# Kernel optimization log

Measured on AMD Instinct MI355X. Metric: run time of the kernel, lower is better.

The kernel has to match this reference:

```python
import jax, jax.numpy as jnp
import numpy as np

B, E, F, Q = 8, 2000, 6000, 20
D = 256   # entity_dim == word_dim (required: word_embedding output feeds LSTM with input_size=word_dim)
WD = 256
L = 3
NUM_ENTITY, NUM_REL, NUM_WORD = 400000, 6000, 60000
NNZ = 2 * B * F
PAGERANK_LAMBDA, FACT_SCALE = 0.8, 3.0
VERY_NEG = -100000000000.0
VERY_SMALL = 1e-10


def _lin(x, W, b):
    return x @ W.T + b


def _sparse_bmm(indices, values, x, num_rows):
    # indices: [3, nnz] = (batch, row, col); x: [B, C, Dx] -> out [B, num_rows, Dx]
    b, r, c = indices[0], indices[1], indices[2]
    contrib = values[:, None] * x[b, c]
    seg = b * num_rows + r
    out = jax.ops.segment_sum(contrib, seg, num_segments=x.shape[0] * num_rows)
    return out.reshape(x.shape[0], num_rows, x.shape[2])


def _lstm(x, Wih, Whh, bih, bhh):
    # PyTorch LSTM, batch_first, 1 layer, unidirectional; gate order i,f,g,o
    Bb, T, _ = x.shape
    H = Whh.shape[1]
    def step(carry, xt):
        h, c = carry
        g = xt @ Wih.T + bih + h @ Whh.T + bhh
        i, f, gg, o = jnp.split(g, 4, axis=-1)
        c = jax.nn.sigmoid(f) * c + jax.nn.sigmoid(i) * jnp.tanh(gg)
        h = jax.nn.sigmoid(o) * jnp.tanh(c)
        return (h, c), h
    init = (jnp.zeros((Bb, H), x.dtype), jnp.zeros((Bb, H), x.dtype))
    (h, c), hs = jax.lax.scan(step, init, jnp.swapaxes(x, 0, 1))
    return jnp.swapaxes(hs, 0, 1), h


def setup_inputs():
    key = jax.random.key(0)
    ks = iter(jax.random.split(key, 48))
    p = lambda shape: jax.random.normal(next(ks), shape, jnp.float32) * 0.02
    inp = {}
    inp['local_entity'] = jax.random.randint(next(ks), (B, E), 0, NUM_ENTITY + 1)
    inp['q2e_adj_mat'] = (jax.random.uniform(next(ks), (B, E, 1)) < 0.01).astype(jnp.float32)
    inp['kb_fact_rel'] = jax.random.randint(next(ks), (B, F), 0, NUM_REL)
    inp['query_text'] = jax.random.randint(next(ks), (B, Q), 0, NUM_WORD)
    inp['answer_dist'] = (jax.random.uniform(next(ks), (B, E)) < 0.005).astype(jnp.float32)
    eb = jax.random.randint(next(ks), (NNZ,), 0, B)
    ef = jax.random.randint(next(ks), (NNZ,), 0, F)
    ee = jax.random.randint(next(ks), (NNZ,), 0, E)
    inp['e2f_indices'] = jnp.stack([eb, ef, ee])
    inp['e2f_val'] = jnp.ones((NNZ,), jnp.float32)
    fb = jax.random.randint(next(ks), (NNZ,), 0, B)
    fe = jax.random.randint(next(ks), (NNZ,), 0, E)
    ff = jax.random.randint(next(ks), (NNZ,), 0, F)
    inp['f2e_indices'] = jnp.stack([fb, fe, ff])
    inp['f2e_val'] = jnp.ones((NNZ,), jnp.float32)
    inp['entity_table'] = p((NUM_ENTITY + 1, WD)).at[-1].set(0.0)
    inp['ent_lin_W'] = p((D, WD)); inp['ent_lin_b'] = jnp.zeros((D,), jnp.float32)
    inp['relation_table'] = p((NUM_REL + 1, WD)).at[-1].set(0.0)
    inp['rel_lin_W'] = p((D, WD)); inp['rel_lin_b'] = jnp.zeros((D,), jnp.float32)
    inp['word_table'] = p((NUM_WORD + 1, D)).at[-1].set(0.0)
    inp['lstm_Wih'] = p((4 * D, WD)); inp['lstm_Whh'] = p((4 * D, D))
    inp['lstm_bih'] = jnp.zeros((4 * D,), jnp.float32); inp['lstm_bhh'] = jnp.zeros((4 * D,), jnp.float32)
    inp['q2e_W'] = p((L, D, D)); inp['q2e_b'] = jnp.zeros((L, D), jnp.float32)
    inp['e2q_W'] = p((L, D, 3 * D)); inp['e2q_b'] = jnp.zeros((L, D), jnp.float32)
    inp['e2e_W'] = p((L, D, 3 * D)); inp['e2e_b'] = jnp.zeros((L, D), jnp.float32)
    inp['head_W'] = p((L, D, D)); inp['head_b'] = jnp.zeros((L, D), jnp.float32)
    inp['tail_W'] = p((L, D, D)); inp['tail_b'] = jnp.zeros((L, D), jnp.float32)
    inp['self_W'] = p((L, D, D)); inp['self_b'] = jnp.zeros((L, D), jnp.float32)
    inp['score_W'] = p((1, D)); inp['score_b'] = jnp.zeros((1,), jnp.float32)
    return inp


def reference(local_entity, q2e_adj_mat, kb_fact_rel, query_text, answer_dist, e2f_indices, e2f_val, f2e_indices, f2e_val, entity_table, ent_lin_W, ent_lin_b, relation_table, rel_lin_W, rel_lin_b, word_table, lstm_Wih, lstm_Whh, lstm_bih, lstm_bhh, q2e_W, q2e_b, e2q_W, e2q_b, e2e_W, e2e_b, head_W, head_b, tail_W, tail_b, self_W, self_b, score_W, score_b):
    query_mask = (query_text != NUM_WORD).astype(jnp.float32)          # [B,Q]
    local_entity_mask = (local_entity != NUM_ENTITY).astype(jnp.float32)
    # query encoder (dropout = identity in eval)
    query_hidden, h_last = _lstm(word_table[query_text], lstm_Wih, lstm_Whh, lstm_bih, lstm_bhh)
    query_node_emb = h_last[:, None, :]                                # [B,1,D]
    local_fact_emb = _lin(relation_table[kb_fact_rel], rel_lin_W, rel_lin_b)  # [B,F,D]
    div = jnp.sqrt(jnp.float32(D))
    sim = jnp.einsum('bqd,bfd->bqf', query_hidden, local_fact_emb) / div
    sim = jax.nn.softmax(sim + (1.0 - query_mask)[:, :, None] * VERY_NEG, axis=1)
    att = jnp.einsum('bqf,bqd->bfd', sim, query_hidden)
    Wt = jnp.sum(att * local_fact_emb, axis=2) / div                   # [B,F]
    W_tilde = jnp.exp(Wt - jnp.max(Wt, axis=1, keepdims=True))
    e2fT = jnp.stack([e2f_indices[0], e2f_indices[2], e2f_indices[1]])  # transpose(1,2)
    e2f_softmax = _sparse_bmm(e2fT, e2f_val, W_tilde[:, :, None], E)[..., 0]
    e2f_softmax = jnp.maximum(e2f_softmax, VERY_SMALL)
    pagerank_f = q2e_adj_mat[..., 0]                                    # [B,E]
    local_entity_emb = _lin(entity_table[local_entity], ent_lin_W, ent_lin_b)  # [B,E,D]
    for i in range(L):
        q2e_emb = jnp.broadcast_to(_lin(query_node_emb, q2e_W[i], q2e_b[i]), (B, E, D))
        nxt = jnp.concatenate([local_entity_emb, q2e_emb], axis=2)
        e2f_emb = jax.nn.relu(_lin(local_fact_emb, self_W[i], self_b[i]) + _sparse_bmm(e2f_indices, e2f_val, _lin(local_entity_emb, head_W[i], head_b[i]), F))
        e2f_norm = W_tilde[:, :, None] * _sparse_bmm(e2f_indices, e2f_val, (pagerank_f / e2f_softmax)[:, :, None], F)
        e2f_emb = e2f_emb * e2f_norm
        f2e_emb = jax.nn.relu(_lin(local_entity_emb, self_W[i], self_b[i]) + _sparse_bmm(f2e_indices, f2e_val, _lin(e2f_emb, tail_W[i], tail_b[i]), E))
        pagerank_f = PAGERANK_LAMBDA * _sparse_bmm(f2e_indices, f2e_val, e2f_norm, E)[..., 0] + (1.0 - PAGERANK_LAMBDA) * pagerank_f
        nxt = jnp.concatenate([nxt, FACT_SCALE * f2e_emb], axis=2)      # [B,E,3D]
        query_node_emb = jnp.einsum('be,bed->bd', pagerank_f, _lin(nxt, e2q_W[i], e2q_b[i]))[:, None, :]
        local_entity_emb = jax.nn.relu(_lin(nxt, e2e_W[i], e2e_b[i]))
    score = _lin(local_entity_emb, score_W, score_b)[..., 0]            # [B,E]
    loss = jnp.mean(jnp.maximum(score, 0.0) - score * answer_dist + jnp.log1p(jnp.exp(-jnp.abs(score))))
    score_m = score + (1.0 - local_entity_mask) * VERY_NEG
    pred = jnp.argmax(score_m, axis=1)
    pred_dist = jax.nn.sigmoid(score_m) * local_entity_mask
    return (loss, pred, pred_dist)
```

## Files before the change

### kernel.cpp

```cpp
#include <hip/hip_runtime.h>
#include <math.h>

#define BB 8
#define EE 2000
#define FF 6000
#define QQ 20
#define DD 256
#define NENT 400000
#define NWORD 60000
#define NNZ_ 96000
#define VNEG  (-1e11f)
#define VSMALL 1e-10f

typedef __attribute__((ext_vector_type(8))) short short8v;
typedef __attribute__((ext_vector_type(4))) short short4v;
typedef __attribute__((ext_vector_type(4))) float f32x4;

__device__ __forceinline__ unsigned short f2bf_rne(float x)
{
    unsigned u = __float_as_uint(x);
    u += 0x7FFFu + ((u >> 16) & 1u);
    return (unsigned short)(u >> 16);
}
__device__ __forceinline__ float bf2f(unsigned short h)
{
    return __uint_as_float((unsigned)h << 16);
}

template<int GATHER, int DUALW, int RELU, int RS, int BIASB>
__device__ __forceinline__ void mgemm_body(
    const float* __restrict__ A1, const int* __restrict__ idx,
    const float* __restrict__ A2, float sA2,
    const short* __restrict__ W1h, const short* __restrict__ W1l,
    const short* __restrict__ W2h, const short* __restrict__ W2l,
    const float* __restrict__ biasA,
    const float* __restrict__ rowscale, const float* __restrict__ bias2,
    float* __restrict__ out, int by, int bx,
    short* __restrict__ Ah, short* __restrict__ Al)
{
    const int tid = threadIdx.x;
    const int lane = tid & 63, wv = tid >> 6;
    const int wrow = wv >> 1, wcol = wv & 1;
    const int row0 = by * 128, col0 = bx * 128;

    const int sr = tid >> 1;
    const int sko = (tid & 1) << 5;
    const int grow = row0 + sr;
    const float* aRow1 = GATHER ? A1 + (size_t)idx[grow] * 256 : A1 + (size_t)grow * 256;
    const float* aRow2 = DUALW ? A2 + (size_t)grow * 256 : nullptr;

    f32x4 acc[4][4];
    #pragma unroll
    for (int i = 0; i < 4; ++i)
        #pragma unroll
        for (int j = 0; j < 4; ++j) acc[i][j] = (f32x4){0.f, 0.f, 0.f, 0.f};

    const int nch = DUALW ? 8 : 4;
    for (int ch = 0; ch < nch; ++ch) {
        const bool hi2 = DUALW && (ch >= 4);
        const float* ar = hi2 ? aRow2 : aRow1;
        const int kbase = (ch & 3) << 6;
        #pragma unroll
        for (int q = 0; q < 8; ++q) {
            const int kc = sko + (q << 2);
            float4 a = *(const float4*)(ar + kbase + kc);
            if (DUALW && hi2) { a.x *= sA2; a.y *= sA2; a.z *= sA2; a.w *= sA2; }
            unsigned short h0 = f2bf_rne(a.x), h1 = f2bf_rne(a.y),
                           h2 = f2bf_rne(a.z), h3 = f2bf_rne(a.w);
            unsigned short l0 = f2bf_rne(a.x - bf2f(h0)), l1 = f2bf_rne(a.y - bf2f(h1)),
                           l2 = f2bf_rne(a.z - bf2f(h2)), l3 = f2bf_rne(a.w - bf2f(h3));
            const int tI = ((sr >> 4) << 1) + (kc >> 5);
            const int off = (tI << 9) + ((((sr & 15)) + (((kc >> 3) & 3) << 4)) << 3) + (kc & 7);
            *(short4v*)(Ah + off) = (short4v){(short)h0, (short)h1, (short)h2, (short)h3};
            *(short4v*)(Al + off) = (short4v){(short)l0, (short)l1, (short)l2, (short)l3};
        }
        __syncthreads();
        const short* Wh = hi2 ? W2h : W1h;
        const short* Wl = hi2 ? W2l : W1l;
        #pragma unroll
        for (int ks = 0; ks < 2; ++ks) {
            const int kg = kbase + (ks << 5) + ((lane >> 4) << 3);
            short8v bh[4], bl[4];
            #pragma unroll
            for (int ct = 0; ct < 4; ++ct) {
                const int c = col0 + (wcol << 6) + (ct << 4) + (lane & 15);
                bh[ct] = *(const short8v*)(Wh + (size_t)c * 256 + kg);
                bl[ct] = *(const short8v*)(Wl + (size_t)c * 256 + kg);
            }
            #pragma unroll
            for (int rt = 0; rt < 4; ++rt) {
                const int tI = (((wrow << 2) + rt) << 1) + ks;
                const short8v avh = *(const short8v*)(Ah + (tI << 9) + (lane << 3));
                const short8v avl = *(const short8v*)(Al + (tI << 9) + (lane << 3));
                #pragma unroll
                for (int ct = 0; ct < 4; ++ct) {
                    acc[rt][ct] = __builtin_amdgcn_mfma_f32_16x16x32_bf16(avh, bh[ct], acc[rt][ct], 0, 0, 0);
                    acc[rt][ct] = __builtin_amdgcn_mfma_f32_16x16x32_bf16(avh, bl[ct], acc[rt][ct], 0, 0, 0);
                    acc[rt][ct] = __builtin_amdgcn_mfma_f32_16x16x32_bf16(avl, bh[ct], acc[rt][ct], 0, 0, 0);
                }
            }
        }
        __syncthreads();
    }
    #pragma unroll
    for (int rt = 0; rt < 4; ++rt) {
        const int rb = row0 + (wrow << 6) + (rt << 4) + ((lane >> 4) << 2);
        #pragma unroll
        for (int ct = 0; ct < 4; ++ct) {
            const int c = col0 + (wcol << 6) + (ct << 4) + (lane & 15);
            #pragma unroll
            for (int j = 0; j < 4; ++j) {
                const int r = rb + j;
                float v = acc[rt][ct][j];
                v += BIASB ? biasA[(size_t)(r / EE) * 256 + c] : biasA[c];
                if (RS) v += rowscale[r] * bias2[c];
                if (RELU) v = fmaxf(v, 0.f);
                out[(size_t)r * 256 + c] = v;
            }
        }
    }
}

template<int GATHER, int DUALW, int RELU, int RS, int BIASB>
__global__ __launch_bounds__(256, 2) void mgemm_k(
    const float* __restrict__ A1, const int* __restrict__ idx,
    const float* __restrict__ A2, float sA2,
    const short* __restrict__ W1h, const short* __restrict__ W1l,
    const short* __restrict__ W2h, const short* __restrict__ W2l,
    const float* __restrict__ biasA,
    const float* __restrict__ rowscale, const float* __restrict__ bias2,
    float* __restrict__ out)
{
    __shared__ short Ah[16 * 512];
    __shared__ short Al[16 * 512];
    mgemm_body<GATHER, DUALW, RELU, RS, BIASB>(A1, idx, A2, sA2, W1h, W1l, W2h, W2l,
        biasA, rowscale, bias2, out, blockIdx.y, blockIdx.x, Ah, Al);
}

template<int GATHER>
__global__ __launch_bounds__(256, 2) void mgemm_pair_k(
    const float* __restrict__ Aa, const int* __restrict__ idxA,
    const short* __restrict__ Wah, const short* __restrict__ Wal,
    const float* __restrict__ ba, float* __restrict__ outa, int nya,
    const float* __restrict__ Ab, const int* __restrict__ idxB,
    const short* __restrict__ Wbh, const short* __restrict__ Wbl,
    const float* __restrict__ bb, float* __restrict__ outb)
{
    __shared__ short Ah[16 * 512];
    __shared__ short Al[16 * 512];
    const int by = blockIdx.y;
    if (by < nya)
        mgemm_body<GATHER, 0, 0, 0, 0>(Aa, idxA, nullptr, 1.f, Wah, Wal, nullptr, nullptr,
            ba, nullptr, nullptr, outa, by, blockIdx.x, Ah, Al);
    else
        mgemm_body<GATHER, 0, 0, 0, 0>(Ab, idxB, nullptr, 1.f, Wbh, Wbl, nullptr, nullptr,
            bb, nullptr, nullptr, outb, by - nya, blockIdx.x, Ah, Al);
}

__global__ void wpack_k(const float* __restrict__ relW, const float* __restrict__ entW,
                        const float* __restrict__ headW, const float* __restrict__ tailW,
                        const float* __restrict__ selfW, const float* __restrict__ e2eW,
                        short* __restrict__ wh, short* __restrict__ wl)
{
    int id = blockIdx.x * 256 + threadIdx.x;
    if (id >= 17 * 65536) return;
    int m = id >> 16, e = id & 65535;
    float x;
    if (m == 0)       x = relW[e];
    else if (m == 1)  x = entW[e];
    else if (m < 5)   x = headW[(size_t)(m - 2) * 65536 + e];
    else if (m < 8)   x = tailW[(size_t)(m - 5) * 65536 + e];
    else if (m < 11)  x = selfW[(size_t)(m - 8) * 65536 + e];
    else if (m < 14)  x = e2eW[(size_t)(m - 11) * 196608 + (size_t)(e >> 8) * 768 + (e & 255)];
    else              x = e2eW[(size_t)(m - 14) * 196608 + (size_t)(e >> 8) * 768 + 512 + (e & 255)];
    unsigned short h = f2bf_rne(x);
    wh[id] = (short)h;
    wl[id] = (short)f2bf_rne(x - bf2f(h));
}

template<int GATHER>
__global__ __launch_bounds__(256, 4) void gemm3_k(
    const float* __restrict__ A1, const int* __restrict__ idx,
    const float* __restrict__ W1, int ldw1,
    const float* __restrict__ biasA,
    float* __restrict__ out, int M, int N)
{
    __shared__ float As[16][68];
    __shared__ float Bs[16][132];
    const int tid = threadIdx.x;
    const int row0 = blockIdx.y * 64, col0 = blockIdx.x * 128;
    const int tx = tid & 15, ty = tid >> 4;
    const int srA = tid >> 2, skA = (tid & 3) << 2;
    const int srB = tid >> 1, skB = (tid & 1) << 3;
    const int grA = row0 + srA;
    const bool rvalid = (grA < M);
    const float* aRow1 = nullptr;
    if (rvalid) aRow1 = GATHER ? A1 + (size_t)idx[grA] * 256 : A1 + (size_t)grA * 256;
    const float* wR1 = W1 + (size_t)(col0 + srB) * ldw1;

    float acc[4][8];
    #pragma unroll
    for (int i = 0; i < 4; ++i)
        #pragma unroll
        for (int j = 0; j < 8; ++j) acc[i][j] = 0.f;

    float4 a0, b0, b1;
    auto fetch = [&](int ch) {
        const int k0 = ch << 4;
        if (rvalid) a0 = *(const float4*)(aRow1 + k0 + skA);
        else        a0 = make_float4(0.f, 0.f, 0.f, 0.f);
        b0 = *(const float4*)(wR1 + k0 + skB);
        b1 = *(const float4*)(wR1 + k0 + skB + 4);
    };

    fetch(0);
    for (int ch = 0; ch < 16; ++ch) {
        As[skA + 0][srA] = a0.x; As[skA + 1][srA] = a0.y;
        As[skA + 2][srA] = a0.z; As[skA + 3][srA] = a0.w;
        Bs[skB + 0][srB] = b0.x; Bs[skB + 1][srB] = b0.y;
        Bs[skB + 2][srB] = b0.z; Bs[skB + 3][srB] = b0.w;
        Bs[skB + 4][srB] = b1.x; Bs[skB + 5][srB] = b1.y;
        Bs[skB + 6][srB] = b1.z; Bs[skB + 7][srB] = b1.w;
        __syncthreads();
        if (ch + 1 < 16) fetch(ch + 1);
        #pragma unroll
        for (int kk = 0; kk < 16; ++kk) {
            float av[4], bv[8];
            *(float4*)&av[0] = *(const float4*)&As[kk][ty << 2];
            *(float4*)&bv[0] = *(const float4*)&Bs[kk][tx << 2];
            *(float4*)&bv[4] = *(const float4*)&Bs[kk][(tx << 2) + 64];
            #pragma unroll
            for (int i = 0; i < 4; ++i)
                #pragma unroll
                for (int j = 0; j < 8; ++j) acc[i][j] += av[i] * bv[j];
        }
        __syncthreads();
    }
    #pragma unroll
    for (int i = 0; i < 4; ++i) {
        int r = row0 + (ty << 2) + i;
        if (r >= M) continue;
        float* orow = out + (size_t)r * N;
        #pragma unroll
        for (int jh = 0; jh < 2; ++jh) {
            const int c = col0 + (jh << 6) + (tx << 2);
            float4 v;
            v.x = acc[i][jh * 4 + 0] + biasA[c + 0];
            v.y = acc[i][jh * 4 + 1] + biasA[c + 1];
            v.z = acc[i][jh * 4 + 2] + biasA[c + 2];
            v.w = acc[i][jh * 4 + 3] + biasA[c + 3];
            *(float4*)(orow + c) = v;
        }
    }
}

__global__ void csr_count2_k(const int* __restrict__ idxA, int* __restrict__ cntA,
                             const int* __restrict__ idxB, int* __restrict__ cntB)
{
    int k = blockIdx.x * 256 + threadIdx.x;
    if (k >= NNZ_) return;
    if (blockIdx.y == 0) atomicAdd(&cntA[idxA[k] * FF + idxA[NNZ_ + k]], 1);
    else                 atomicAdd(&cntB[idxB[k] * EE + idxB[NNZ_ + k]], 1);
}

__global__ __launch_bounds__(1024) void scan2_k(
    const int* __restrict__ cntA, int* __restrict__ rpA, int* __restrict__ curA, int nA,
    const int* __restrict__ cntB, int* __restrict__ rpB, int* __restrict__ curB, int nB)
{
    const int* cnt = blockIdx.x ? cntB : cntA;
    int* rp  = blockIdx.x ? rpB  : rpA;
    int* cur = blockIdx.x ? curB : curA;
    int n    = blockIdx.x ? nB   : nA;
    __shared__ int sums[1024];
    int t = threadIdx.x;
    int chunk = (n + 1023) / 1024;
    int lo = t * chunk, hi = lo + chunk;
    if (lo > n) lo = n;
    if (hi > n) hi = n;
    int s = 0;
    for (int i = lo; i < hi; ++i) s += cnt[i];
    sums[t] = s;
    __syncthreads();
    for (int off = 1; off < 1024; off <<= 1) {
        int v = (t >= off) ? sums[t - off] : 0;
        __syncthreads();
        sums[t] += v;
        __syncthreads();
    }
    int run = (t == 0) ? 0 : sums[t - 1];
    for (int i = lo; i < hi; ++i) { rp[i] = run; cur[i] = run; run += cnt[i]; }
    if (hi == n) rp[n] = run;
}

__global__ void csr_fill2_k(
    const int* __restrict__ idxA, const float* __restrict__ valA,
    int* __restrict__ curA, int* __restrict__ colA, float* __restrict__ vpA,
    const int* __restrict__ idxB, const float* __restrict__ valB,
    int* __restrict__ curB, int* __restrict__ colB, float* __restrict__ vpB)
{
    int k = blockIdx.x * 256 + threadIdx.x;
    if (k >= NNZ_) return;
    if (blockIdx.y == 0) {
        int row = idxA[k] * FF + idxA[NNZ_ + k];
        int p = atomicAdd(&curA[row], 1);
        colA[p] = idxA[2 * NNZ_ + k];
        vpA[p] = valA[k];
    } else {
        int row = idxB[k] * EE + idxB[NNZ_ + k];
        int p = atomicAdd(&curB[row], 1);
        colB[p] = idxB[2 * NNZ_ + k];
        vpB[p] = valB[k];
    }
}

__global__ void degw_k(const int* __restrict__ rp, const float* __restrict__ vp,
                       float* __restrict__ degw, int n)
{
    int r = blockIdx.x * 256 + threadIdx.x;
    if (r >= n) return;
    float s = 0.f;
    for (int j = rp[r]; j < rp[r + 1]; ++j) s += vp[j];
    degw[r] = s;
}

__global__ __launch_bounds__(256) void gather_fused_e2f_k(
    const int* __restrict__ rowptr, const int* __restrict__ col,
    const float* __restrict__ valp, const float* __restrict__ headsrc,
    const float* __restrict__ pr, const float* __restrict__ sm,
    const float* __restrict__ Wtil, float* __restrict__ e2fnrm,
    float* __restrict__ dst, int nrows)
{
    int gid = blockIdx.x * 256 + threadIdx.x;
    int row = gid >> 6, lane = gid & 63;
    if (row >= nrows) return;
    int b = row / FF;
    const float* prb = pr + (size_t)b * EE;
    const float* smb = sm + (size_t)b * EE;
    float4* dp = (float4*)(dst + (size_t)row * DD + (lane << 2));
    float4 acc = *dp;
    float ns = 0.f;
    int j0 = rowptr[row], j1 = rowptr[row + 1];
    for (int j = j0; j < j1; ++j) {
        int c = col[j];
        float v = valp[j];
        float4 x = *(const float4*)(headsrc + ((size_t)b * EE + c) * DD + (lane << 2));
        acc.x += v * x.x; acc.y += v * x.y; acc.z += v * x.z; acc.w += v * x.w;
        ns += v * (prb[c] / fmaxf(smb[c], VSMALL));
    }
    float nrm = Wtil[row] * ns;
    if (lane == 0) e2fnrm[row] = nrm;
    acc.x = fmaxf(acc.x, 0.f) * nrm; acc.y = fmaxf(acc.y, 0.f) * nrm;
    acc.z = fmaxf(acc.z, 0.f) * nrm; acc.w = fmaxf(acc.w, 0.f) * nrm;
    *dp = acc;
}

__global__ __launch_bounds__(256) void gather_sum_k(
    const int* __restrict__ rowptr, const int* __restrict__ col,
    const float* __restrict__ valp, const float* __restrict__ src,
    float* __restrict__ dst, int nrows, int nrPerB, int ncs)
{
    int gid = blockIdx.x * 256 + threadIdx.x;
    int row = gid >> 6, lane = gid & 63;
    if (row >= nrows) return;
    int b = row / nrPerB;
    float4 acc = make_float4(0.f, 0.f, 0.f, 0.f);
    int j0 = rowptr[row], j1 = rowptr[row + 1];
    for (int j = j0; j < j1; ++j) {
        int c = col[j];
        float v = valp[j];
        float4 x = *(const float4*)(src + ((size_t)b * ncs + c) * DD + (lane << 2));
        acc.x += v * x.x; acc.y += v * x.y; acc.z += v * x.z; acc.w += v * x.w;
    }
    *(float4*)(dst + (size_t)row * DD + (lane << 2)) = acc;
}

__global__ void transpose_whh_k(const float* __restrict__ Whh, float* __restrict__ WhhT)
{
    int i = blockIdx.x * 256 + threadIdx.x;
    int k = i >> 10, j = i & 1023;
    WhhT[i] = Whh[(size_t)j * 256 + k];
}

__global__ __launch_bounds__(256) void lstm_k(
    const float* __restrict__ Xg, const float* __restrict__ WhhT,
    const float* __restrict__ bhh, float* __restrict__ qh, float* __restrict__ qne)
{
    __shared__ float h[DD];
    __shared__ float gs[4 * DD];
    const int b = blockIdx.x, t = threadIdx.x;
    h[t] = 0.f;
    float c = 0.f;
    const float4 bb4 = *(const float4*)(bhh + 4 * t);
    const float4* wt4 = (const float4*)WhhT + t;
    __syncthreads();
    for (int step = 0; step < QQ; ++step) {
        float a0 = 0.f, a1 = 0.f, a2 = 0.f, a3 = 0.f;
        #pragma unroll 16
        for (int k = 0; k < DD; ++k) {
            float4 w = wt4[k * 256];
            float hk = h[k];
            a0 += w.x * hk; a1 += w.y * hk; a2 += w.z * hk; a3 += w.w * hk;
        }
        float4 xg = *(const float4*)(Xg + ((size_t)b * QQ + step) * 1024 + 4 * t);
        float4 g4 = make_float4(a0 + xg.x + bb4.x, a1 + xg.y + bb4.y,
                                a2 + xg.z + bb4.z, a3 + xg.w + bb4.w);
        *(float4*)(gs + 4 * t) = g4;
        __syncthreads();
        float gi = gs[t], gf = gs[DD + t], gg = gs[2 * DD + t], go = gs[3 * DD + t];
        float si = 1.f / (1.f + expf(-gi));
        float sf = 1.f / (1.f + expf(-gf));
        float so = 1.f / (1.f + expf(-go));
        c = sf * c + si * tanhf(gg);
        float hh = so * tanhf(c);
        h[t] = hh;
        qh[((size_t)b * QQ + step) * DD + t] = hh;
        __syncthreads();
    }
    qne[(size_t)b * DD + t] = h[t];
}

__global__ __launch_bounds__(256) void simwt_k(
    const float* __restrict__ qhid, const int* __restrict__ qtext,
    const float* __restrict__ lfe, float* __restrict__ Wt)
{
    __shared__ float qs[QQ * DD];
    __shared__ float qmn[QQ];
    const int b = blockIdx.y;
    const int f = blockIdx.x * 256 + threadIdx.x;
    for (int i = threadIdx.x; i < QQ * DD; i += 256) qs[i] = qhid[(size_t)b * QQ * DD + i];
    if (threadIdx.x < QQ)
        qmn[threadIdx.x] = (qtext[b * QQ + threadIdx.x] != NWORD) ? 0.f : VNEG;
    __syncthreads();
    if (f >= FF) return;
    float acc[QQ];
    #pragma unroll
    for (int q = 0; q < QQ; ++q) acc[q] = 0.f;
    const float* lr = lfe + ((size_t)b * FF + f) * DD;
    for (int d = 0; d < DD; d += 4) {
        float4 x = *(const float4*)(lr + d);
        #pragma unroll
        for (int q = 0; q < QQ; ++q) {
            float4 y = *(const float4*)&qs[q * DD + d];
            acc[q] += x.x * y.x + x.y * y.y + x.z * y.z + x.w * y.w;
        }
    }
    const float inv = 0.0625f;
    float pre[QQ], m = -INFINITY;
    #pragma unroll
    for (int q = 0; q < QQ; ++q) { pre[q] = acc[q] * inv + qmn[q]; m = fmaxf(m, pre[q]); }
    float s = 0.f;
    #pragma unroll
    for (int q = 0; q < QQ; ++q) s += expf(pre[q] - m);
    float wt = 0.f;
    #pragma unroll
    for (int q = 0; q < QQ; ++q) wt += (expf(pre[q] - m) / s) * (acc[q] * inv);
    Wt[(size_t)b * FF + f] = wt;
}

__global__ __launch_bounds__(256) void rowmax_wtil_k(
    const float* __restrict__ Wt, float* __restrict__ Wtil)
{
    __shared__ float red[256];
    int b = blockIdx.x, t = threadIdx.x;
    float m = -INFINITY;
    for (int f = t; f < FF; f += 256) m = fmaxf(m, Wt[b * FF + f]);
    red[t] = m; __syncthreads();
    for (int s = 128; s > 0; s >>= 1) {
        if (t < s) red[t] = fmaxf(red[t], red[t + s]);
        __syncthreads();
    }
    float mx = red[0];
    for (int f = t; f < FF; f += 256) Wtil[b * FF + f] = expf(Wt[b * FF + f] - mx);
}

__global__ void scatter_sm_k(const int* __restrict__ idx, const float* __restrict__ val,
                             const float* __restrict__ Wtil, float* __restrict__ dst)
{
    int k = blockIdx.x * 256 + threadIdx.x;
    if (k >= NNZ_) return;
    int b = idx[k], e = idx[2 * NNZ_ + k], f = idx[NNZ_ + k];
    atomicAdd(&dst[(size_t)b * EE + e], val[k] * Wtil[(size_t)b * FF + f]);
}

__global__ __launch_bounds__(256) void qlin_ebias_k(
    const float* __restrict__ qne, const float* __restrict__ q2eW,
    const float* __restrict__ q2eb, const float* __restrict__ e2eW,
    const float* __restrict__ e2eb, float* __restrict__ qlin, float* __restrict__ ebias)
{
    __shared__ float xs[DD], qs[DD];
    int b = blockIdx.x, j = threadIdx.x;
    xs[j] = qne[b * DD + j];
    __syncthreads();
    float acc = q2eb[j];
    const float* wr = q2eW + (size_t)j * DD;
    #pragma unroll 4
    for (int k = 0; k < DD; ++k) acc += xs[k] * wr[k];
    qlin[b * DD + j] = acc;
    qs[j] = acc;
    __syncthreads();
    float acc2 = e2eb[j];
    const float* wr2 = e2eW + (size_t)j * 768 + 256;
    #pragma unroll 4
    for (int k = 0; k < DD; ++k) acc2 += qs[k] * wr2[k];
    ebias[b * DD + j] = acc2;
}

#define VCH 80
#define NCHK (EE / VCH)
__global__ __launch_bounds__(256) void vreduce_pr_k(
    const int* __restrict__ f2e_rp, const int* __restrict__ f2e_col,
    const float* __restrict__ f2e_vp, const float* __restrict__ e2fnrm,
    float* __restrict__ pr, const float* __restrict__ lee,
    const float* __restrict__ f2e, float* __restrict__ vpartL,
    float* __restrict__ vpartF, float* __restrict__ vpartS)
{
    int b = blockIdx.y, ch = blockIdx.x, k = threadIdx.x;
    int e0 = ch * VCH;
    __shared__ float prs[VCH];
    if (k < VCH) {
        int row = b * EE + e0 + k;
        float s = 0.f;
        for (int j = f2e_rp[row]; j < f2e_rp[row + 1]; ++j)
            s += f2e_vp[j] * e2fnrm[(size_t)b * FF + f2e_col[j]];
        float v = 0.8f * s + 0.2f * pr[row];
        pr[row] = v;
        prs[k] = v;
    }
    __syncthreads();
    float a1 = 0.f, a2 = 0.f;
    for (int e = 0; e < VCH; ++e) {
        float p = prs[e];
        size_t base = ((size_t)b * EE + e0 + e) * DD + k;
        a1 += p * lee[base];
        a2 += p * f2e[base];
    }
    int pi = ch * BB + b;
    vpartL[(size_t)pi * DD + k] = a1;
    vpartF[(size_t)pi * DD + k] = a2;
    float sp = 0.f;
    for (int e = k; e < VCH; e += 256) sp += prs[e];
    __shared__ float red[256];
    red[k] = sp; __syncthreads();
    for (int s = 128; s > 0; s >>= 1) {
        if (k < s) red[k] += red[k + s];
        __syncthreads();
    }
    if (k == 0) vpartS[pi] = red[0];
}

__global__ __launch_bounds__(256) void qneupd_qlin_k(
    const float* __restrict__ vpartL, const float* __restrict__ vpartF,
    const float* __restrict__ vpartS, const float* __restrict__ qlinCur,
    const float* __restrict__ W, const float* __restrict__ bias,
    float* __restrict__ qne,
    const float* __restrict__ q2eWn, const float* __restrict__ q2ebn,
    const float* __restrict__ e2eWn, const float* __restrict__ e2ebn,
    float* __restrict__ qlinNext, float* __restrict__ ebiasNext, int hasNext)
{
    __shared__ float s1[DD], s2[DD], s3[DD], qn[DD], qs[DD];
    int b = blockIdx.x, j = threadIdx.x;
    float a1 = 0.f, a3 = 0.f, sp = 0.f;
    for (int ch = 0; ch < NCHK; ++ch) {
        int pi = ch * BB + b;
        a1 += vpartL[(size_t)pi * DD + j];
        a3 += vpartF[(size_t)pi * DD + j];
        sp += vpartS[pi];
    }
    s1[j] = a1; s2[j] = qlinCur[b * DD + j]; s3[j] = a3;
    __syncthreads();
    float acc = sp * bias[j];
    const float* wr = W + (size_t)j * 768;
    #pragma unroll 4
    for (int k = 0; k < DD; ++k)
        acc += s1[k] * wr[k] + sp * s2[k] * wr[256 + k] + 3.f * s3[k] * wr[512 + k];
    qne[b * DD + j] = acc;
    if (!hasNext) return;
    qn[j] = acc;
    __syncthreads();
    float aq = q2ebn[j];
    const float* wq = q2eWn + (size_t)j * DD;
    #pragma unroll 4
    for (int k = 0; k < DD; ++k) aq += qn[k] * wq[k];
    qlinNext[b * DD + j] = aq;
    qs[j] = aq;
    __syncthreads();
    float ae = e2ebn[j];
    const float* we = e2eWn + (size_t)j * 768 + 256;
    #pragma unroll 4
    for (int k = 0; k < DD; ++k) ae += qs[k] * we[k];
    ebiasNext[b * DD + j] = ae;
}

__global__ __launch_bounds__(256) void final2_k(
    const float* __restrict__ lee, const float* __restrict__ sw_,
    const float* __restrict__ sb, const int* __restrict__ local_entity,
    const float* __restrict__ ans, float* __restrict__ out, float* __restrict__ losspart)
{
    __shared__ float sw[DD];
    int b = blockIdx.x, t = threadIdx.x;
    sw[t] = sw_[t];
    __syncthreads();
    float sb0 = sb[0];
    float lsum = 0.f, bm = -INFINITY;
    int bi = EE;
    for (int e = t; e < EE; e += 256) {
        const float* a = lee + ((size_t)b * EE + e) * DD;
        float s = sb0;
        for (int k = 0; k < DD; k += 4) {
            float4 v = *(const float4*)(a + k);
            s += v.x * sw[k] + v.y * sw[k + 1] + v.z * sw[k + 2] + v.w * sw[k + 3];
        }
        float mask = (local_entity[b * EE + e] != NENT) ? 1.f : 0.f;
        float smv = s + (1.f - mask) * VNEG;
        float sig;
        if (smv >= 0.f) sig = 1.f / (1.f + expf(-smv));
        else { float es = expf(smv); sig = es / (1.f + es); }
        out[1 + BB + b * EE + e] = sig * mask;
        lsum += fmaxf(s, 0.f) - s * ans[b * EE + e] + log1pf(expf(-fabsf(s)));
        if (smv > bm) { bm = smv; bi = e; }
    }
    __shared__ float rv[256]; __shared__ int ri[256]; __shared__ float rl[256];
    rv[t] = bm; ri[t] = bi; rl[t] = lsum;
    __syncthreads();
    for (int s = 128; s > 0; s >>= 1) {
        if (t < s) {
            rl[t] += rl[t + s];
            if (rv[t + s] > rv[t] || (rv[t + s] == rv[t] && ri[t + s] < ri[t])) {
                rv[t] = rv[t + s]; ri[t] = ri[t + s];
            }
        }
        __syncthreads();
    }
    if (t == 0) { losspart[b] = rl[0]; out[1 + b] = (float)ri[0]; }
}

__global__ void loss_k(const float* __restrict__ losspart, float* __restrict__ out)
{
    if (threadIdx.x == 0) {
        float s = 0.f;
        for (int b = 0; b < BB; ++b) s += losspart[b];
        out[0] = s / (float)(BB * EE);
    }
}

extern "C" void kernel_launch(void* const* d_in, const int* in_sizes, int n_in,
                              void* d_out, int out_size, void* d_ws, size_t ws_size,
                              hipStream_t stream)
{
    (void)in_sizes; (void)n_in; (void)out_size; (void)ws_size;
    const int*   local_entity = (const int*)d_in[0];
    const float* q2e_adj      = (const float*)d_in[1];
    const int*   kb_fact_rel  = (const int*)d_in[2];
    const int*   query_text   = (const int*)d_in[3];
    const float* answer_dist  = (const float*)d_in[4];
    const int*   e2f_idx      = (const int*)d_in[5];
    const float* e2f_val      = (const float*)d_in[6];
    const int*   f2e_idx      = (const int*)d_in[7];
    const float* f2e_val      = (const float*)d_in[8];
    const float* entity_table = (const float*)d_in[9];
    const float* ent_W        = (const float*)d_in[10];
    const float* ent_b        = (const float*)d_in[11];
    const float* rel_table    = (const float*)d_in[12];
    const float* rel_W        = (const float*)d_in[13];
    const float* rel_b        = (const float*)d_in[14];
    const float* word_table   = (const float*)d_in[15];
    const float* Wih          = (const float*)d_in[16];
    const float* Whh          = (const float*)d_in[17];
    const float* bih          = (const float*)d_in[18];
    const float* bhh          = (const float*)d_in[19];
    const float* q2e_W        = (const float*)d_in[20];
    const float* q2e_b        = (const float*)d_in[21];
    const float* e2q_W        = (const float*)d_in[22];
    const float* e2q_b        = (const float*)d_in[23];
    const float* e2e_W        = (const float*)d_in[24];
    const float* e2e_b        = (const float*)d_in[25];
    const float* head_W       = (const float*)d_in[26];
    const float* head_b       = (const float*)d_in[27];
    const float* tail_W       = (const float*)d_in[28];
    const float* tail_b       = (const float*)d_in[29];
    const float* self_W       = (const float*)d_in[30];
    const float* self_b       = (const float*)d_in[31];
    const float* score_W      = (const float*)d_in[32];
    const float* score_b      = (const float*)d_in[33];

    const int NR1 = BB * FF;
    const int NR2 = BB * EE;

    float* ws = (float*)d_ws;
    size_t off = 0;
    auto alloc = [&](size_t n) { float* p = ws + off; off += n; return p; };
    auto salloc = [&](size_t nshorts) { short* p = (short*)(ws + off); off += nshorts / 2; return p; };
    float* Xg      = alloc((size_t)BB * QQ * 1024);
    float* WhhT    = alloc((size_t)1024 * DD);
    float* qh      = alloc((size_t)BB * QQ * DD);
    float* qne     = alloc(BB * DD);
    float* lfe     = alloc((size_t)NR1 * DD);
    float* leeA    = alloc((size_t)NR2 * DD);
    float* leeB    = alloc((size_t)NR2 * DD);
    float* Wt      = alloc(BB * FF);
    float* Wtil    = alloc(BB * FF);
    float* e2fsm   = alloc(BB * EE);
    float* pr      = alloc(BB * EE);
    float* qlinA   = alloc(BB * DD);
    float* qlinB   = alloc(BB * DD);
    float* ebiasA  = alloc(BB * DD);
    float* ebiasB  = alloc(BB * DD);
    float* e2fnrm  = alloc(BB * FF);
    float* losspart= alloc(8);
    float* bufC    = alloc((size_t)NR2 * DD);
    float* e2fT    = alloc((size_t)NR1 * DD);
    float* f2eT    = alloc((size_t)NR2 * DD);
    float* tmp     = alloc((size_t)NR2 * DD);
    float* vpartL  = alloc((size_t)NCHK * BB * DD);
    float* vpartF  = alloc((size_t)NCHK * BB * DD);
    float* vpartS  = alloc(NCHK * BB);
    float* degw2   = alloc(NR2);
    float* e2f_vp  = alloc(NNZ_);
    float* f2e_vp  = alloc(NNZ_);
    short* wbh     = salloc((size_t)17 * 65536);
    short* wbl     = salloc((size_t)17 * 65536);
    int* ib = (int*)(ws + off);
    size_t ioff = 0;
    auto ialloc = [&](size_t n) { int* p = ib + ioff; ioff += n; return p; };
    int* e2f_cnt = ialloc(NR1);
    int* e2f_rp  = ialloc(NR1 + 1);
    int* e2f_cur = ialloc(NR1);
    int* e2f_col = ialloc(NNZ_);
    int* f2e_cnt = ialloc(NR2);
    int* f2e_rp  = ialloc(NR2 + 1);
    int* f2e_cur = ialloc(NR2);
    int* f2e_col = ialloc(NNZ_);

    auto WH = [&](int m) { return wbh + (size_t)m * 65536; };
    auto WL = [&](int m) { return wbl + (size_t)m * 65536; };

    float* outp = (float*)d_out;
    const int SCB = (NNZ_ + 255) / 256;

    wpack_k<<<(17 * 65536) / 256, 256, 0, stream>>>(rel_W, ent_W, head_W, tail_W,
                                                    self_W, e2e_W, wbh, wbl);

    hipMemsetAsync(e2f_cnt, 0, NR1 * sizeof(int), stream);
    hipMemsetAsync(f2e_cnt, 0, NR2 * sizeof(int), stream);
    csr_count2_k<<<dim3(SCB, 2), 256, 0, stream>>>(e2f_idx, e2f_cnt, f2e_idx, f2e_cnt);
    scan2_k<<<2, 1024, 0, stream>>>(e2f_cnt, e2f_rp, e2f_cur, NR1,
                                    f2e_cnt, f2e_rp, f2e_cur, NR2);
    csr_fill2_k<<<dim3(SCB, 2), 256, 0, stream>>>(
        e2f_idx, e2f_val, e2f_cur, e2f_col, e2f_vp,
        f2e_idx, f2e_val, f2e_cur, f2e_col, f2e_vp);
    degw_k<<<(NR2 + 255) / 256, 256, 0, stream>>>(f2e_rp, f2e_vp, degw2, NR2);

    gemm3_k<1><<<dim3(8, 3), 256, 0, stream>>>(
        word_table, query_text, Wih, 256, bih, Xg, BB * QQ, 1024);
    transpose_whh_k<<<1024, 256, 0, stream>>>(Whh, WhhT);
    lstm_k<<<BB, 256, 0, stream>>>(Xg, WhhT, bhh, qh, qne);

    mgemm_pair_k<1><<<dim3(2, 375 + 125), 256, 0, stream>>>(
        rel_table, kb_fact_rel, WH(0), WL(0), rel_b, lfe, 375,
        entity_table, local_entity, WH(1), WL(1), ent_b, leeA);

    simwt_k<<<dim3((FF + 255) / 256, BB), 256, 0, stream>>>(qh, query_text, lfe, Wt);
    rowmax_wtil_k<<<BB, 256, 0, stream>>>(Wt, Wtil);

    hipMemsetAsync(e2fsm, 0, BB * EE * sizeof(float), stream);
    scatter_sm_k<<<SCB, 256, 0, stream>>>(e2f_idx, e2f_val, Wtil, e2fsm);

    hipMemcpyAsync(pr, q2e_adj, BB * EE * sizeof(float), hipMemcpyDeviceToDevice, stream);
    qlin_ebias_k<<<BB, 256, 0, stream>>>(qne, q2e_W, q2e_b, e2e_W, e2e_b, qlinA, ebiasA);

    float* lee = leeA;   float* lee2 = leeB;
    float* qlinCur = qlinA;  float* qlinNxt = qlinB;
    float* ebiasCur = ebiasA; float* ebiasNxt = ebiasB;

    for (int i = 0; i < 3; ++i) {
        const float* e2qWi  = e2q_W  + (size_t)i * DD * 3 * DD;
        const float* e2qbi  = e2q_b  + i * DD;
        const float* headbi = head_b + i * DD;
        const float* tailbi = tail_b + i * DD;
        const float* selfbi = self_b + i * DD;

        mgemm_pair_k<0><<<dim3(2, 125 + 375), 256, 0, stream>>>(
            lee, nullptr, WH(2 + i), WL(2 + i), headbi, bufC, 125,
            lfe, nullptr, WH(8 + i), WL(8 + i), selfbi, e2fT);

        gather_fused_e2f_k<<<(NR1 * 64) / 256, 256, 0, stream>>>(
            e2f_rp, e2f_col, e2f_vp, bufC, pr, e2fsm, Wtil, e2fnrm, e2fT, NR1);

        gather_sum_k<<<(NR2 * 64) / 256, 256, 0, stream>>>(
            f2e_rp, f2e_col, f2e_vp, e2fT, tmp, NR2, EE, FF);

        mgemm_k<0, 1, 1, 1, 0><<<dim3(2, 125), 256, 0, stream>>>(
            lee, nullptr, tmp, 1.f, WH(8 + i), WL(8 + i), WH(5 + i), WL(5 + i),
            selfbi, degw2, tailbi, f2eT);

        vreduce_pr_k<<<dim3(NCHK, BB), 256, 0, stream>>>(
            f2e_rp, f2e_col, f2e_vp, e2fnrm, pr, lee, f2eT, vpartL, vpartF, vpartS);

        int hasNext = (i < 2) ? 1 : 0;
        const float* q2eWn = q2e_W + (size_t)(i + 1) * DD * DD * (hasNext ? 1 : 0);
        const float* q2ebn = q2e_b + (i + 1) * DD * (hasNext ? 1 : 0);
        const float* e2eWn = e2e_W + (size_t)(i + 1) * DD * 3 * DD * (hasNext ? 1 : 0);
        const float* e2ebn = e2e_b + (i + 1) * DD * (hasNext ? 1 : 0);
        qneupd_qlin_k<<<BB, 256, 0, stream>>>(
            vpartL, vpartF, vpartS, qlinCur, e2qWi, e2qbi, qne,
            q2eWn, q2ebn, e2eWn, e2ebn, qlinNxt, ebiasNxt, hasNext);

        mgemm_k<0, 1, 1, 0, 1><<<dim3(2, 125), 256, 0, stream>>>(
            lee, nullptr, f2eT, 3.f, WH(11 + i), WL(11 + i), WH(14 + i), WL(14 + i),
            ebiasCur, nullptr, nullptr, lee2);
        { float* t = lee; lee = lee2; lee2 = t; }
        { float* t = qlinCur; qlinCur = qlinNxt; qlinNxt = t; }
        { float* t = ebiasCur; ebiasCur = ebiasNxt; ebiasNxt = t; }
    }

    final2_k<<<BB, 256, 0, stream>>>(lee, score_W, score_b, local_entity,
                                     answer_dist, outp, losspart);
    loss_k<<<1, 64, 0, stream>>>(losspart, outp);
}
```

Measured before the change: 1.295 ms.

## Store activations as pre-split bf16 hi/lo and fuse small kernels into GEMM launches

GEMM epilogues now also write the bf16 hi/lo split of their outputs, so the next GEMM can load pre-split A tiles instead of converting fp32 on every tile load. The small per-batch kernels (qlin/ebias, qne update, vreduce/pagerank) are folded into the grids of the large GEMM launches as extra blocks, and the 3x scale is moved into the packed e2e weights. This cuts repeated conversion work and the number of kernel launches across the layer loop. In exchange it adds workspace for the split copies and extra epilogue stores, and the cross-layer schedule is reshuffled (the qne update is delayed to the next layer's launch).

```diff
diff --git a/kernel.cpp b/kernel.cpp
--- a/kernel.cpp
+++ b/kernel.cpp
@@ -27,16 +27,17 @@
     return __uint_as_float((unsigned)h << 16);
 }
 
-template<int GATHER, int DUALW, int RELU, int RS, int BIASB>
+template<int GATHER, int ASPLIT, int DUALW, int RELU, int RS, int BIASB, int WRITEB>
 __device__ __forceinline__ void mgemm_body(
-    const float* __restrict__ A1, const int* __restrict__ idx,
-    const float* __restrict__ A2, float sA2,
+    const float* __restrict__ A1f, const int* __restrict__ idx,
+    const short* __restrict__ A1h, const short* __restrict__ A1l,
+    const short* __restrict__ A2h, const short* __restrict__ A2l,
     const short* __restrict__ W1h, const short* __restrict__ W1l,
     const short* __restrict__ W2h, const short* __restrict__ W2l,
     const float* __restrict__ biasA,
     const float* __restrict__ rowscale, const float* __restrict__ bias2,
-    float* __restrict__ out, int by, int bx,
-    short* __restrict__ Ah, short* __restrict__ Al)
+    float* __restrict__ outF, short* __restrict__ outH, short* __restrict__ outL,
+    int by, int bx, short* __restrict__ Ah, short* __restrict__ Al)
 {
     const int tid = threadIdx.x;
     const int lane = tid & 63, wv = tid >> 6;
@@ -46,8 +47,9 @@
     const int sr = tid >> 1;
     const int sko = (tid & 1) << 5;
     const int grow = row0 + sr;
-    const float* aRow1 = GATHER ? A1 + (size_t)idx[grow] * 256 : A1 + (size_t)grow * 256;
-    const float* aRow2 = DUALW ? A2 + (size_t)grow * 256 : nullptr;
+    const float* aRowF = nullptr;
+    if (!ASPLIT) aRowF = GATHER ? A1f + (size_t)idx[grow] * 256 : A1f + (size_t)grow * 256;
+    const size_t arow = (size_t)grow * 256;
 
     f32x4 acc[4][4];
     #pragma unroll
@@ -58,21 +60,34 @@
     const int nch = DUALW ? 8 : 4;
     for (int ch = 0; ch < nch; ++ch) {
         const bool hi2 = DUALW && (ch >= 4);
-        const float* ar = hi2 ? aRow2 : aRow1;
         const int kbase = (ch & 3) << 6;
-        #pragma unroll
-        for (int q = 0; q < 8; ++q) {
-            const int kc = sko + (q << 2);
-            float4 a = *(const float4*)(ar + kbase + kc);
-            if (DUALW && hi2) { a.x *= sA2; a.y *= sA2; a.z *= sA2; a.w *= sA2; }
-            unsigned short h0 = f2bf_rne(a.x), h1 = f2bf_rne(a.y),
-                           h2 = f2bf_rne(a.z), h3 = f2bf_rne(a.w);
-            unsigned short l0 = f2bf_rne(a.x - bf2f(h0)), l1 = f2bf_rne(a.y - bf2f(h1)),
-                           l2 = f2bf_rne(a.z - bf2f(h2)), l3 = f2bf_rne(a.w - bf2f(h3));
-            const int tI = ((sr >> 4) << 1) + (kc >> 5);
-            const int off = (tI << 9) + ((((sr & 15)) + (((kc >> 3) & 3) << 4)) << 3) + (kc & 7);
-            *(short4v*)(Ah + off) = (short4v){(short)h0, (short)h1, (short)h2, (short)h3};
-            *(short4v*)(Al + off) = (short4v){(short)l0, (short)l1, (short)l2, (short)l3};
+        if (ASPLIT) {
+            const short* __restrict__ sH = (hi2 ? A2h : A1h) + arow + kbase + sko;
+            const short* __restrict__ sL = (hi2 ? A2l : A1l) + arow + kbase + sko;
+            #pragma unroll
+            for (int q = 0; q < 4; ++q) {
+                const int kc = sko + (q << 3);
+                short8v h = *(const short8v*)(sH + (q << 3));
+                short8v l = *(const short8v*)(sL + (q << 3));
+                const int tI = ((sr >> 4) << 1) + (kc >> 5);
+                const int off = (tI << 9) + (((sr & 15) + (((kc >> 3) & 3) << 4)) << 3);
+                *(short8v*)(Ah + off) = h;
+                *(short8v*)(Al + off) = l;
+            }
+        } else {
+            #pragma unroll
+            for (int q = 0; q < 8; ++q) {
+                const int kc = sko + (q << 2);
+                float4 a = *(const float4*)(aRowF + kbase + kc);
+                unsigned short h0 = f2bf_rne(a.x), h1 = f2bf_rne(a.y),
+                               h2 = f2bf_rne(a.z), h3 = f2bf_rne(a.w);
+                unsigned short l0 = f2bf_rne(a.x - bf2f(h0)), l1 = f2bf_rne(a.y - bf2f(h1)),
+                               l2 = f2bf_rne(a.z - bf2f(h2)), l3 = f2bf_rne(a.w - bf2f(h3));
+                const int tI = ((sr >> 4) << 1) + (kc >> 5);
+                const int off = (tI << 9) + (((sr & 15) + (((kc >> 3) & 3) << 4)) << 3) + (kc & 7);
+                *(short4v*)(Ah + off) = (short4v){(short)h0, (short)h1, (short)h2, (short)h3};
+                *(short4v*)(Al + off) = (short4v){(short)l0, (short)l1, (short)l2, (short)l3};
+            }
         }
         __syncthreads();
         const short* Wh = hi2 ? W2h : W1h;
@@ -115,46 +130,236 @@
                 v += BIASB ? biasA[(size_t)(r / EE) * 256 + c] : biasA[c];
                 if (RS) v += rowscale[r] * bias2[c];
                 if (RELU) v = fmaxf(v, 0.f);
-                out[(size_t)r * 256 + c] = v;
+                outF[(size_t)r * 256 + c] = v;
+                if (WRITEB) {
+                    unsigned short h = f2bf_rne(v);
+                    outH[(size_t)r * 256 + c] = (short)h;
+                    outL[(size_t)r * 256 + c] = (short)f2bf_rne(v - bf2f(h));
+                }
             }
         }
     }
 }
 
-template<int GATHER, int DUALW, int RELU, int RS, int BIASB>
-__global__ __launch_bounds__(256, 2) void mgemm_k(
-    const float* __restrict__ A1, const int* __restrict__ idx,
-    const float* __restrict__ A2, float sA2,
+__device__ __forceinline__ void qlin_ebias_body(
+    int b, int j, const float* __restrict__ qne, const float* __restrict__ q2eW,
+    const float* __restrict__ q2eb, const float* __restrict__ e2eW,
+    const float* __restrict__ e2eb, float* __restrict__ qlin,
+    float* __restrict__ ebias, float* __restrict__ lds)
+{
+    float* xs = lds; float* qs = lds + 256;
+    xs[j] = qne[b * DD + j];
+    __syncthreads();
+    float acc = q2eb[j];
+    const float* wr = q2eW + (size_t)j * DD;
+    #pragma unroll 4
+    for (int k = 0; k < DD; ++k) acc += xs[k] * wr[k];
+    qlin[b * DD + j] = acc;
+    qs[j] = acc;
+    __syncthreads();
+    float acc2 = e2eb[j];
+    const float* wr2 = e2eW + (size_t)j * 768 + 256;
+    #pragma unroll 4
+    for (int k = 0; k < DD; ++k) acc2 += qs[k] * wr2[k];
+    ebias[b * DD + j] = acc2;
+}
+
+#define VCH 80
+#define NCHK (EE / VCH)
+__device__ __forceinline__ void qneupd_body(
+    int b, int j, const float* __restrict__ vpartL, const float* __restrict__ vpartF,
+    const float* __restrict__ vpartS, const float* __restrict__ qlinCur,
+    const float* __restrict__ W, const float* __restrict__ bias,
+    float* __restrict__ qne,
+    const float* __restrict__ q2eWn, const float* __restrict__ q2ebn,
+    const float* __restrict__ e2eWn, const float* __restrict__ e2ebn,
+    float* __restrict__ qlinNext, float* __restrict__ ebiasNext,
+    float* __restrict__ lds)
+{
+    float* s1 = lds; float* s2 = lds + 256; float* s3 = lds + 512;
+    float* qn = lds + 768; float* qs = lds + 1024;
+    float a1 = 0.f, a3 = 0.f, sp = 0.f;
+    for (int ch = 0; ch < NCHK; ++ch) {
+        int pi = ch * BB + b;
+        a1 += vpartL[(size_t)pi * DD + j];
+        a3 += vpartF[(size_t)pi * DD + j];
+        sp += vpartS[pi];
+    }
+    s1[j] = a1; s2[j] = qlinCur[b * DD + j]; s3[j] = a3;
+    __syncthreads();
+    float acc = sp * bias[j];
+    const float* wr = W + (size_t)j * 768;
+    #pragma unroll 4
+    for (int k = 0; k < DD; ++k)
+        acc += s1[k] * wr[k] + sp * s2[k] * wr[256 + k] + 3.f * s3[k] * wr[512 + k];
+    qne[b * DD + j] = acc;
+    qn[j] = acc;
+    __syncthreads();
+    float aq = q2ebn[j];
+    const float* wq = q2eWn + (size_t)j * DD;
+    #pragma unroll 4
+    for (int k = 0; k < DD; ++k) aq += qn[k] * wq[k];
+    qlinNext[b * DD + j] = aq;
+    qs[j] = aq;
+    __syncthreads();
+    float ae = e2ebn[j];
+    const float* we = e2eWn + (size_t)j * 768 + 256;
+    #pragma unroll 4
+    for (int k = 0; k < DD; ++k) ae += qs[k] * we[k];
+    ebiasNext[b * DD + j] = ae;
+}
+
+__device__ __forceinline__ void vreduce_body(
+    int ch, int b, int k,
+    const int* __restrict__ f2e_rp, const int* __restrict__ f2e_col,
+    const float* __restrict__ f2e_vp, const float* __restrict__ e2fnrm,
+    float* __restrict__ pr, const float* __restrict__ lee,
+    const float* __restrict__ f2e, float* __restrict__ vpartL,
+    float* __restrict__ vpartF, float* __restrict__ vpartS,
+    float* __restrict__ lds)
+{
+    float* prs = lds; float* red = lds + 128;
+    int e0 = ch * VCH;
+    if (k < VCH) {
+        int row = b * EE + e0 + k;
+        float s = 0.f;
+        for (int j = f2e_rp[row]; j < f2e_rp[row + 1]; ++j)
+            s += f2e_vp[j] * e2fnrm[(size_t)b * FF + f2e_col[j]];
+        float v = 0.8f * s + 0.2f * pr[row];
+        pr[row] = v;
+        prs[k] = v;
+    }
+    __syncthreads();
+    float a1 = 0.f, a2 = 0.f;
+    for (int e = 0; e < VCH; ++e) {
+        float p = prs[e];
+        size_t base = ((size_t)b * EE + e0 + e) * DD + k;
+        a1 += p * lee[base];
+        a2 += p * f2e[base];
+    }
+    int pi = ch * BB + b;
+    vpartL[(size_t)pi * DD + k] = a1;
+    vpartF[(size_t)pi * DD + k] = a2;
+    float sp = 0.f;
+    for (int e = k; e < VCH; e += 256) sp += prs[e];
+    red[k] = sp; __syncthreads();
+    for (int s = 128; s > 0; s >>= 1) {
+        if (k < s) red[k] += red[k + s];
+        __syncthreads();
+    }
+    if (k == 0) vpartS[pi] = red[0];
+}
+
+__global__ __launch_bounds__(256, 2) void embed_pair_k(
+    const float* __restrict__ rel_table, const int* __restrict__ kb_fact_rel,
+    const short* __restrict__ W0h, const short* __restrict__ W0l,
+    const float* __restrict__ rel_b, float* __restrict__ lfe,
+    short* __restrict__ lfeH, short* __restrict__ lfeL,
+    const float* __restrict__ ent_table, const int* __restrict__ local_entity,
     const short* __restrict__ W1h, const short* __restrict__ W1l,
-    const short* __restrict__ W2h, const short* __restrict__ W2l,
-    const float* __restrict__ biasA,
-    const float* __restrict__ rowscale, const float* __restrict__ bias2,
-    float* __restrict__ out)
-{
-    __shared__ short Ah[16 * 512];
-    __shared__ short Al[16 * 512];
-    mgemm_body<GATHER, DUALW, RELU, RS, BIASB>(A1, idx, A2, sA2, W1h, W1l, W2h, W2l,
-        biasA, rowscale, bias2, out, blockIdx.y, blockIdx.x, Ah, Al);
-}
-
-template<int GATHER>
-__global__ __launch_bounds__(256, 2) void mgemm_pair_k(
-    const float* __restrict__ Aa, const int* __restrict__ idxA,
-    const short* __restrict__ Wah, const short* __restrict__ Wal,
-    const float* __restrict__ ba, float* __restrict__ outa, int nya,
-    const float* __restrict__ Ab, const int* __restrict__ idxB,
-    const short* __restrict__ Wbh, const short* __restrict__ Wbl,
-    const float* __restrict__ bb, float* __restrict__ outb)
-{
-    __shared__ short Ah[16 * 512];
-    __shared__ short Al[16 * 512];
-    const int by = blockIdx.y;
-    if (by < nya)
-        mgemm_body<GATHER, 0, 0, 0, 0>(Aa, idxA, nullptr, 1.f, Wah, Wal, nullptr, nullptr,
-            ba, nullptr, nullptr, outa, by, blockIdx.x, Ah, Al);
-    else
-        mgemm_body<GATHER, 0, 0, 0, 0>(Ab, idxB, nullptr, 1.f, Wbh, Wbl, nullptr, nullptr,
-            bb, nullptr, nullptr, outb, by - nya, blockIdx.x, Ah, Al);
+    const float* __restrict__ ent_b, float* __restrict__ lee,
+    short* __restrict__ leeH, short* __restrict__ leeL,
+    const float* __restrict__ qne, const float* __restrict__ q2eW,
+    const float* __restrict__ q2eb, const float* __restrict__ e2eW,
+    const float* __restrict__ e2eb, float* __restrict__ qlin, float* __restrict__ ebias)
+{
+    __shared__ char ldsbuf[32768];
+    int blk = blockIdx.x;
+    if (blk < 1000) {
+        short* Ah = (short*)ldsbuf; short* Al = Ah + 8192;
+        int bx = blk & 1, by = blk >> 1;
+        if (by < 375)
+            mgemm_body<1, 0, 0, 0, 0, 0, 1>(rel_table, kb_fact_rel, nullptr, nullptr,
+                nullptr, nullptr, W0h, W0l, nullptr, nullptr, rel_b, nullptr, nullptr,
+                lfe, lfeH, lfeL, by, bx, Ah, Al);
+        else
+            mgemm_body<1, 0, 0, 0, 0, 0, 1>(ent_table, local_entity, nullptr, nullptr,
+                nullptr, nullptr, W1h, W1l, nullptr, nullptr, ent_b, nullptr, nullptr,
+                lee, leeH, leeL, by - 375, bx, Ah, Al);
+    } else {
+        qlin_ebias_body(blk - 1000, threadIdx.x, qne, q2eW, q2eb, e2eW, e2eb,
+                        qlin, ebias, (float*)ldsbuf);
+    }
+}
+
+template<int NQ>
+__global__ __launch_bounds__(256, 2) void layer_pair_k(
+    const short* __restrict__ leeH, const short* __restrict__ leeL,
+    const short* __restrict__ lfeH, const short* __restrict__ lfeL,
+    const short* __restrict__ WheadH, const short* __restrict__ WheadL,
+    const short* __restrict__ WselfH, const short* __restrict__ WselfL,
+    const float* __restrict__ headb, const float* __restrict__ selfb,
+    float* __restrict__ bufC, float* __restrict__ e2fT,
+    const float* __restrict__ vpartL, const float* __restrict__ vpartF,
+    const float* __restrict__ vpartS, const float* __restrict__ qlinCur,
+    const float* __restrict__ e2qW, const float* __restrict__ e2qb,
+    float* __restrict__ qne,
+    const float* __restrict__ q2eWn, const float* __restrict__ q2ebn,
+    const float* __restrict__ e2eWn, const float* __restrict__ e2ebn,
+    float* __restrict__ qlinNext, float* __restrict__ ebiasNext)
+{
+    __shared__ char ldsbuf[32768];
+    int blk = blockIdx.x;
+    if (blk < 1000) {
+        short* Ah = (short*)ldsbuf; short* Al = Ah + 8192;
+        int bx = blk & 1, by = blk >> 1;
+        if (by < 125)
+            mgemm_body<0, 1, 0, 0, 0, 0, 0>(nullptr, nullptr, leeH, leeL, nullptr, nullptr,
+                WheadH, WheadL, nullptr, nullptr, headb, nullptr, nullptr,
+                bufC, nullptr, nullptr, by, bx, Ah, Al);
+        else
+            mgemm_body<0, 1, 0, 0, 0, 0, 0>(nullptr, nullptr, lfeH, lfeL, nullptr, nullptr,
+                WselfH, WselfL, nullptr, nullptr, selfb, nullptr, nullptr,
+                e2fT, nullptr, nullptr, by - 125, bx, Ah, Al);
+    } else if (NQ) {
+        qneupd_body(blk - 1000, threadIdx.x, vpartL, vpartF, vpartS, qlinCur,
+                    e2qW, e2qb, qne, q2eWn, q2ebn, e2eWn, e2ebn,
+                    qlinNext, ebiasNext, (float*)ldsbuf);
+    }
+}
+
+__global__ __launch_bounds__(256, 2) void f2et_k(
+    const short* __restrict__ leeH, const short* __restrict__ leeL,
+    const short* __restrict__ tmpH, const short* __restrict__ tmpL,
+    const short* __restrict__ WselfH, const short* __restrict__ WselfL,
+    const short* __restrict__ WtailH, const short* __restrict__ WtailL,
+    const float* __restrict__ selfb, const float* __restrict__ degw,
+    const float* __restrict__ tailb,
+    float* __restrict__ f2eT, short* __restrict__ f2eH, short* __restrict__ f2eL)
+{
+    __shared__ char ldsbuf[32768];
+    short* Ah = (short*)ldsbuf; short* Al = Ah + 8192;
+    mgemm_body<0, 1, 1, 1, 1, 0, 1>(nullptr, nullptr, leeH, leeL, tmpH, tmpL,
+        WselfH, WselfL, WtailH, WtailL, selfb, degw, tailb,
+        f2eT, f2eH, f2eL, blockIdx.y, blockIdx.x, Ah, Al);
+}
+
+template<int DOV>
+__global__ __launch_bounds__(256, 2) void tail_k(
+    const short* __restrict__ leeH, const short* __restrict__ leeL,
+    const short* __restrict__ f2eH, const short* __restrict__ f2eL,
+    const short* __restrict__ WaH, const short* __restrict__ WaL,
+    const short* __restrict__ WbH, const short* __restrict__ WbL,
+    const float* __restrict__ ebias, float* __restrict__ lee2,
+    short* __restrict__ lee2H, short* __restrict__ lee2L,
+    const int* __restrict__ f2e_rp, const int* __restrict__ f2e_col,
+    const float* __restrict__ f2e_vp, const float* __restrict__ e2fnrm,
+    float* __restrict__ pr, const float* __restrict__ lee,
+    const float* __restrict__ f2eT, float* __restrict__ vpartL,
+    float* __restrict__ vpartF, float* __restrict__ vpartS)
+{
+    __shared__ char ldsbuf[32768];
+    int blk = blockIdx.x;
+    if (blk < 250) {
+        short* Ah = (short*)ldsbuf; short* Al = Ah + 8192;
+        mgemm_body<0, 1, 1, 1, 0, 1, 1>(nullptr, nullptr, leeH, leeL, f2eH, f2eL,
+            WaH, WaL, WbH, WbL, ebias, nullptr, nullptr,
+            lee2, lee2H, lee2L, blk >> 1, blk & 1, Ah, Al);
+    } else if (DOV) {
+        int v = blk - 250;
+        vreduce_body(v >> 3, v & 7, threadIdx.x, f2e_rp, f2e_col, f2e_vp, e2fnrm,
+                     pr, lee, f2eT, vpartL, vpartF, vpartS, (float*)ldsbuf);
+    }
 }
 
 __global__ void wpack_k(const float* __restrict__ relW, const float* __restrict__ entW,
@@ -172,13 +377,12 @@
     else if (m < 8)   x = tailW[(size_t)(m - 5) * 65536 + e];
     else if (m < 11)  x = selfW[(size_t)(m - 8) * 65536 + e];
     else if (m < 14)  x = e2eW[(size_t)(m - 11) * 196608 + (size_t)(e >> 8) * 768 + (e & 255)];
-    else              x = e2eW[(size_t)(m - 14) * 196608 + (size_t)(e >> 8) * 768 + 512 + (e & 255)];
+    else              x = 3.f * e2eW[(size_t)(m - 14) * 196608 + (size_t)(e >> 8) * 768 + 512 + (e & 255)];
     unsigned short h = f2bf_rne(x);
     wh[id] = (short)h;
     wl[id] = (short)f2bf_rne(x - bf2f(h));
 }
 
-template<int GATHER>
 __global__ __launch_bounds__(256, 4) void gemm3_k(
     const float* __restrict__ A1, const int* __restrict__ idx,
     const float* __restrict__ W1, int ldw1,
@@ -195,7 +399,7 @@
     const int grA = row0 + srA;
     const bool rvalid = (grA < M);
     const float* aRow1 = nullptr;
-    if (rvalid) aRow1 = GATHER ? A1 + (size_t)idx[grA] * 256 : A1 + (size_t)grA * 256;
+    if (rvalid) aRow1 = A1 + (size_t)idx[grA] * 256;
     const float* wR1 = W1 + (size_t)(col0 + srB) * ldw1;
 
     float acc[4][8];
@@ -354,10 +558,10 @@
     *dp = acc;
 }
 
-__global__ __launch_bounds__(256) void gather_sum_k(
+__global__ __launch_bounds__(256) void gather_sum_bf_k(
     const int* __restrict__ rowptr, const int* __restrict__ col,
     const float* __restrict__ valp, const float* __restrict__ src,
-    float* __restrict__ dst, int nrows, int nrPerB, int ncs)
+    short* __restrict__ dh, short* __restrict__ dl, int nrows, int nrPerB, int ncs)
 {
     int gid = blockIdx.x * 256 + threadIdx.x;
     int row = gid >> 6, lane = gid & 63;
@@ -371,7 +575,13 @@
         float4 x = *(const float4*)(src + ((size_t)b * ncs + c) * DD + (lane << 2));
         acc.x += v * x.x; acc.y += v * x.y; acc.z += v * x.z; acc.w += v * x.w;
     }
-    *(float4*)(dst + (size_t)row * DD + (lane << 2)) = acc;
+    unsigned short h0 = f2bf_rne(acc.x), h1 = f2bf_rne(acc.y),
+                   h2 = f2bf_rne(acc.z), h3 = f2bf_rne(acc.w);
+    size_t o = (size_t)row * DD + (lane << 2);
+    *(short4v*)(dh + o) = (short4v){(short)h0, (short)h1, (short)h2, (short)h3};
+    *(short4v*)(dl + o) = (short4v){
+        (short)f2bf_rne(acc.x - bf2f(h0)), (short)f2bf_rne(acc.y - bf2f(h1)),
+        (short)f2bf_rne(acc.z - bf2f(h2)), (short)f2bf_rne(acc.w - bf2f(h3))};
 }
 
 __global__ void transpose_whh_k(const float* __restrict__ Whh, float* __restrict__ WhhT)
@@ -480,115 +690,6 @@
     if (k >= NNZ_) return;
     int b = idx[k], e = idx[2 * NNZ_ + k], f = idx[NNZ_ + k];
     atomicAdd(&dst[(size_t)b * EE + e], val[k] * Wtil[(size_t)b * FF + f]);
-}
-
-__global__ __launch_bounds__(256) void qlin_ebias_k(
-    const float* __restrict__ qne, const float* __restrict__ q2eW,
-    const float* __restrict__ q2eb, const float* __restrict__ e2eW,
-    const float* __restrict__ e2eb, float* __restrict__ qlin, float* __restrict__ ebias)
-{
-    __shared__ float xs[DD], qs[DD];
-    int b = blockIdx.x, j = threadIdx.x;
-    xs[j] = qne[b * DD + j];
-    __syncthreads();
-    float acc = q2eb[j];
-    const float* wr = q2eW + (size_t)j * DD;
-    #pragma unroll 4
-    for (int k = 0; k < DD; ++k) acc += xs[k] * wr[k];
-    qlin[b * DD + j] = acc;
-    qs[j] = acc;
-    __syncthreads();
-    float acc2 = e2eb[j];
-    const float* wr2 = e2eW + (size_t)j * 768 + 256;
-    #pragma unroll 4
-    for (int k = 0; k < DD; ++k) acc2 += qs[k] * wr2[k];
-    ebias[b * DD + j] = acc2;
-}
-
-#define VCH 80
-#define NCHK (EE / VCH)
-__global__ __launch_bounds__(256) void vreduce_pr_k(
-    const int* __restrict__ f2e_rp, const int* __restrict__ f2e_col,
-    const float* __restrict__ f2e_vp, const float* __restrict__ e2fnrm,
-    float* __restrict__ pr, const float* __restrict__ lee,
-    const float* __restrict__ f2e, float* __restrict__ vpartL,
-    float* __restrict__ vpartF, float* __restrict__ vpartS)
-{
-    int b = blockIdx.y, ch = blockIdx.x, k = threadIdx.x;
-    int e0 = ch * VCH;
-    __shared__ float prs[VCH];
-    if (k < VCH) {
-        int row = b * EE + e0 + k;
-        float s = 0.f;
-        for (int j = f2e_rp[row]; j < f2e_rp[row + 1]; ++j)
-            s += f2e_vp[j] * e2fnrm[(size_t)b * FF + f2e_col[j]];
-        float v = 0.8f * s + 0.2f * pr[row];
-        pr[row] = v;
-        prs[k] = v;
-    }
-    __syncthreads();
-    float a1 = 0.f, a2 = 0.f;
-    for (int e = 0; e < VCH; ++e) {
-        float p = prs[e];
-        size_t base = ((size_t)b * EE + e0 + e) * DD + k;
-        a1 += p * lee[base];
-        a2 += p * f2e[base];
-    }
-    int pi = ch * BB + b;
-    vpartL[(size_t)pi * DD + k] = a1;
-    vpartF[(size_t)pi * DD + k] = a2;
-    float sp = 0.f;
-    for (int e = k; e < VCH; e += 256) sp += prs[e];
-    __shared__ float red[256];
-    red[k] = sp; __syncthreads();
-    for (int s = 128; s > 0; s >>= 1) {
-        if (k < s) red[k] += red[k + s];
-        __syncthreads();
-    }
-    if (k == 0) vpartS[pi] = red[0];
-}
-
-__global__ __launch_bounds__(256) void qneupd_qlin_k(
-    const float* __restrict__ vpartL, const float* __restrict__ vpartF,
-    const float* __restrict__ vpartS, const float* __restrict__ qlinCur,
-    const float* __restrict__ W, const float* __restrict__ bias,
-    float* __restrict__ qne,
-    const float* __restrict__ q2eWn, const float* __restrict__ q2ebn,
-    const float* __restrict__ e2eWn, const float* __restrict__ e2ebn,
-    float* __restrict__ qlinNext, float* __restrict__ ebiasNext, int hasNext)
-{
-    __shared__ float s1[DD], s2[DD], s3[DD], qn[DD], qs[DD];
-    int b = blockIdx.x, j = threadIdx.x;
-    float a1 = 0.f, a3 = 0.f, sp = 0.f;
-    for (int ch = 0; ch < NCHK; ++ch) {
-        int pi = ch * BB + b;
-        a1 += vpartL[(size_t)pi * DD + j];
-        a3 += vpartF[(size_t)pi * DD + j];
-        sp += vpartS[pi];
-    }
-    s1[j] = a1; s2[j] = qlinCur[b * DD + j]; s3[j] = a3;
-    __syncthreads();
-    float acc = sp * bias[j];
-    const float* wr = W + (size_t)j * 768;
-    #pragma unroll 4
-    for (int k = 0; k < DD; ++k)
-        acc += s1[k] * wr[k] + sp * s2[k] * wr[256 + k] + 3.f * s3[k] * wr[512 + k];
-    qne[b * DD + j] = acc;
-    if (!hasNext) return;
-    qn[j] = acc;
-    __syncthreads();
-    float aq = q2ebn[j];
-    const float* wq = q2eWn + (size_t)j * DD;
-    #pragma unroll 4
-    for (int k = 0; k < DD; ++k) aq += qn[k] * wq[k];
-    qlinNext[b * DD + j] = aq;
-    qs[j] = aq;
-    __syncthreads();
-    float ae = e2ebn[j];
-    const float* we = e2eWn + (size_t)j * 768 + 256;
-    #pragma unroll 4
-    for (int k = 0; k < DD; ++k) ae += qs[k] * we[k];
-    ebiasNext[b * DD + j] = ae;
 }
 
 __global__ __launch_bounds__(256) void final2_k(
@@ -689,7 +790,7 @@
     float* ws = (float*)d_ws;
     size_t off = 0;
     auto alloc = [&](size_t n) { float* p = ws + off; off += n; return p; };
-    auto salloc = [&](size_t nshorts) { short* p = (short*)(ws + off); off += nshorts / 2; return p; };
+    auto salloc = [&](size_t nshorts) { short* p = (short*)(ws + off); off += (nshorts + 1) / 2; return p; };
     float* Xg      = alloc((size_t)BB * QQ * 1024);
     float* WhhT    = alloc((size_t)1024 * DD);
     float* qh      = alloc((size_t)BB * QQ * DD);
@@ -710,15 +811,24 @@
     float* bufC    = alloc((size_t)NR2 * DD);
     float* e2fT    = alloc((size_t)NR1 * DD);
     float* f2eT    = alloc((size_t)NR2 * DD);
-    float* tmp     = alloc((size_t)NR2 * DD);
     float* vpartL  = alloc((size_t)NCHK * BB * DD);
     float* vpartF  = alloc((size_t)NCHK * BB * DD);
     float* vpartS  = alloc(NCHK * BB);
     float* degw2   = alloc(NR2);
     float* e2f_vp  = alloc(NNZ_);
     float* f2e_vp  = alloc(NNZ_);
-    short* wbh     = salloc((size_t)17 * 65536);
-    short* wbl     = salloc((size_t)17 * 65536);
+    short* lfeH  = salloc((size_t)NR1 * DD);
+    short* lfeL  = salloc((size_t)NR1 * DD);
+    short* leeHA = salloc((size_t)NR2 * DD);
+    short* leeLA = salloc((size_t)NR2 * DD);
+    short* leeHB = salloc((size_t)NR2 * DD);
+    short* leeLB = salloc((size_t)NR2 * DD);
+    short* f2eH  = salloc((size_t)NR2 * DD);
+    short* f2eL  = salloc((size_t)NR2 * DD);
+    short* tmpH  = salloc((size_t)NR2 * DD);
+    short* tmpL  = salloc((size_t)NR2 * DD);
+    short* wbh   = salloc((size_t)17 * 65536);
+    short* wbl   = salloc((size_t)17 * 65536);
     int* ib = (int*)(ws + off);
     size_t ioff = 0;
     auto ialloc = [&](size_t n) { int* p = ib + ioff; ioff += n; return p; };
@@ -750,14 +860,15 @@
         f2e_idx, f2e_val, f2e_cur, f2e_col, f2e_vp);
     degw_k<<<(NR2 + 255) / 256, 256, 0, stream>>>(f2e_rp, f2e_vp, degw2, NR2);
 
-    gemm3_k<1><<<dim3(8, 3), 256, 0, stream>>>(
+    gemm3_k<<<dim3(8, 3), 256, 0, stream>>>(
         word_table, query_text, Wih, 256, bih, Xg, BB * QQ, 1024);
     transpose_whh_k<<<1024, 256, 0, stream>>>(Whh, WhhT);
     lstm_k<<<BB, 256, 0, stream>>>(Xg, WhhT, bhh, qh, qne);
 
-    mgemm_pair_k<1><<<dim3(2, 375 + 125), 256, 0, stream>>>(
-        rel_table, kb_fact_rel, WH(0), WL(0), rel_b, lfe, 375,
-        entity_table, local_entity, WH(1), WL(1), ent_b, leeA);
+    embed_pair_k<<<1008, 256, 0, stream>>>(
+        rel_table, kb_fact_rel, WH(0), WL(0), rel_b, lfe, lfeH, lfeL,
+        entity_table, local_entity, WH(1), WL(1), ent_b, leeA, leeHA, leeLA,
+        qne, q2e_W, q2e_b, e2e_W, e2e_b, qlinA, ebiasA);
 
     simwt_k<<<dim3((FF + 255) / 256, BB), 256, 0, stream>>>(qh, query_text, lfe, Wt);
     rowmax_wtil_k<<<BB, 256, 0, stream>>>(Wt, Wtil);
@@ -766,51 +877,66 @@
     scatter_sm_k<<<SCB, 256, 0, stream>>>(e2f_idx, e2f_val, Wtil, e2fsm);
 
     hipMemcpyAsync(pr, q2e_adj, BB * EE * sizeof(float), hipMemcpyDeviceToDevice, stream);
-    qlin_ebias_k<<<BB, 256, 0, stream>>>(qne, q2e_W, q2e_b, e2e_W, e2e_b, qlinA, ebiasA);
 
     float* lee = leeA;   float* lee2 = leeB;
+    short* leeH = leeHA; short* leeL = leeLA;
+    short* leeH2 = leeHB; short* leeL2 = leeLB;
     float* qlinCur = qlinA;  float* qlinNxt = qlinB;
     float* ebiasCur = ebiasA; float* ebiasNxt = ebiasB;
 
     for (int i = 0; i < 3; ++i) {
-        const float* e2qWi  = e2q_W  + (size_t)i * DD * 3 * DD;
-        const float* e2qbi  = e2q_b  + i * DD;
         const float* headbi = head_b + i * DD;
         const float* tailbi = tail_b + i * DD;
         const float* selfbi = self_b + i * DD;
 
-        mgemm_pair_k<0><<<dim3(2, 125 + 375), 256, 0, stream>>>(
-            lee, nullptr, WH(2 + i), WL(2 + i), headbi, bufC, 125,
-            lfe, nullptr, WH(8 + i), WL(8 + i), selfbi, e2fT);
+        if (i == 0) {
+            layer_pair_k<0><<<1000, 256, 0, stream>>>(
+                leeH, leeL, lfeH, lfeL, WH(2 + i), WL(2 + i), WH(8 + i), WL(8 + i),
+                headbi, selfbi, bufC, e2fT,
+                nullptr, nullptr, nullptr, nullptr, nullptr, nullptr, nullptr,
+                nullptr, nullptr, nullptr, nullptr, nullptr, nullptr);
+        } else {
+            const float* e2qWp = e2q_W + (size_t)(i - 1) * DD * 3 * DD;
+            const float* e2qbp = e2q_b + (i - 1) * DD;
+            const float* q2eWn = q2e_W + (size_t)i * DD * DD;
+            const float* q2ebn = q2e_b + i * DD;
+            const float* e2eWn = e2e_W + (size_t)i * DD * 3 * DD;
+            const float* e2ebn = e2e_b + i * DD;
+            layer_pair_k<1><<<1008, 256, 0, stream>>>(
+                leeH, leeL, lfeH, lfeL, WH(2 + i), WL(2 + i), WH(8 + i), WL(8 + i),
+                headbi, selfbi, bufC, e2fT,
+                vpartL, vpartF, vpartS, qlinCur, e2qWp, e2qbp, qne,
+                q2eWn, q2ebn, e2eWn, e2ebn, qlinNxt, ebiasNxt);
+            { float* t = qlinCur; qlinCur = qlinNxt; qlinNxt = t; }
+            { float* t = ebiasCur; ebiasCur = ebiasNxt; ebiasNxt = t; }
+        }
 
         gather_fused_e2f_k<<<(NR1 * 64) / 256, 256, 0, stream>>>(
             e2f_rp, e2f_col, e2f_vp, bufC, pr, e2fsm, Wtil, e2fnrm, e2fT, NR1);
 
-        gather_sum_k<<<(NR2 * 64) / 256, 256, 0, stream>>>(
-            f2e_rp, f2e_col, f2e_vp, e2fT, tmp, NR2, EE, FF);
-
-        mgemm_k<0, 1, 1, 1, 0><<<dim3(2, 125), 256, 0, stream>>>(
-            lee, nullptr, tmp, 1.f, WH(8 + i), WL(8 + i), WH(5 + i), WL(5 + i),
-            selfbi, degw2, tailbi, f2eT);
-
-        vreduce_pr_k<<<dim3(NCHK, BB), 256, 0, stream>>>(
-            f2e_rp, f2e_col, f2e_vp, e2fnrm, pr, lee, f2eT, vpartL, vpartF, vpartS);
-
-        int hasNext = (i < 2) ? 1 : 0;
-        const float* q2eWn = q2e_W + (size_t)(i + 1) * DD * DD * (hasNext ? 1 : 0);
-        const float* q2ebn = q2e_b + (i + 1) * DD * (hasNext ? 1 : 0);
-        const float* e2eWn = e2e_W + (size_t)(i + 1) * DD * 3 * DD * (hasNext ? 1 : 0);
-        const float* e2ebn = e2e_b + (i + 1) * DD * (hasNext ? 1 : 0);
-        qneupd_qlin_k<<<BB, 256, 0, stream>>>(
-            vpartL, vpartF, vpartS, qlinCur, e2qWi, e2qbi, qne,
-            q2eWn, q2ebn, e2eWn, e2ebn, qlinNxt, ebiasNxt, hasNext);
-
-        mgemm_k<0, 1, 1, 0, 1><<<dim3(2, 125), 256, 0, stream>>>(
-            lee, nullptr, f2eT, 3.f, WH(11 + i), WL(11 + i), WH(14 + i), WL(14 + i),
-            ebiasCur, nullptr, nullptr, lee2);
+        gather_sum_bf_k<<<(NR2 * 64) / 256, 256, 0, stream>>>(
+            f2e_rp, f2e_col, f2e_vp, e2fT, tmpH, tmpL, NR2, EE, FF);
+
+        f2et_k<<<dim3(2, 125), 256, 0, stream>>>(
+            leeH, leeL, tmpH, tmpL, WH(8 + i), WL(8 + i), WH(5 + i), WL(5 + i),
+            selfbi, degw2, tailbi, f2eT, f2eH, f2eL);
+
+        if (i < 2) {
+            tail_k<1><<<450, 256, 0, stream>>>(
+                leeH, leeL, f2eH, f2eL, WH(11 + i), WL(11 + i), WH(14 + i), WL(14 + i),
+                ebiasCur, lee2, leeH2, leeL2,
+                f2e_rp, f2e_col, f2e_vp, e2fnrm, pr, lee, f2eT,
+                vpartL, vpartF, vpartS);
+        } else {
+            tail_k<0><<<250, 256, 0, stream>>>(
+                leeH, leeL, f2eH, f2eL, WH(11 + i), WL(11 + i), WH(14 + i), WL(14 + i),
+                ebiasCur, lee2, leeH2, leeL2,
+                f2e_rp, f2e_col, f2e_vp, e2fnrm, pr, lee, f2eT,
+                vpartL, vpartF, vpartS);
+        }
         { float* t = lee; lee = lee2; lee2 = t; }
-        { float* t = qlinCur; qlinCur = qlinNxt; qlinNxt = t; }
-        { float* t = ebiasCur; ebiasCur = ebiasNxt; ebiasNxt = t; }
+        { short* t = leeH; leeH = leeH2; leeH2 = t; }
+        { short* t = leeL; leeL = leeL2; leeL2 = t; }
     }
 
     final2_k<<<BB, 256, 0, stream>>>(lee, score_W, score_b, local_entity,
```

After: 1.338 ms. +3.3%, slower.
